# Kernel tuning notes

Hardware: AMD Instinct MI355X
Metric: run time of the kernel (lower is better)

Reference implementation:

```python
import jax, jax.numpy as jnp
import numpy as np

NUM_HEADS = 16
NEG_INF = -1e30


def setup_inputs() -> dict:
    key = jax.random.key(0)
    k1, k2, k3 = jax.random.split(key, 3)
    B, S, D = 2, 2048, 1024
    x = jax.random.normal(k1, (B, S, D), dtype=jnp.float32)
    # torch Linear(D, 3D, bias=False) stored here already transposed: y = x @ w_qkv
    w_qkv = jax.random.normal(k2, (D, 3 * D), dtype=jnp.float32) * 0.02
    w_out = jax.random.normal(k3, (D, D), dtype=jnp.float32) * 0.02
    return {"x": x, "w_qkv": w_qkv, "w_out": w_out}


def reference(x, w_qkv, w_out):
    B, S, D = x.shape
    H = NUM_HEADS
    dh = D // H
    qkv = x @ w_qkv                      # [B, S, 3D]
    q, k, v = jnp.split(qkv, 3, axis=-1)

    def to_heads(t):
        return t.reshape(B, S, H, dh).transpose(0, 2, 1, 3)  # [B, H, S, dh]

    q, k, v = to_heads(q), to_heads(k), to_heads(v)
    scale = jnp.asarray(dh, x.dtype) ** -0.5
    scores = jnp.einsum('bhqd,bhkd->bhqk', q, k) * scale     # [B, H, S, S]
    causal = jnp.tril(jnp.ones((S, S), dtype=bool))
    scores = jnp.where(causal, scores, NEG_INF)
    attn = jax.nn.softmax(scores, axis=-1)
    out = jnp.einsum('bhqk,bhkd->bhqd', attn, v)             # [B, H, S, dh]
    out = out.transpose(0, 2, 1, 3).reshape(B, S, D)
    return out @ w_out
```

## Files before the change

### kernel.cpp

```cpp
#include <hip/hip_runtime.h>

typedef unsigned short u16;
typedef unsigned int u32;

typedef __bf16 bf16x8 __attribute__((ext_vector_type(8)));
typedef _Float16 f16x8 __attribute__((ext_vector_type(8)));
typedef float f32x4 __attribute__((ext_vector_type(4)));

typedef __attribute__((address_space(1))) u32 as1_u32;
typedef __attribute__((address_space(3))) u32 as3_u32;

#define EKF 0.18033688011112042f

__device__ __forceinline__ u16 f2bf(float x) {
  u32 u = __float_as_uint(x);
  u = u + 0x7fffu + ((u >> 16) & 1u);
  return (u16)(u >> 16);
}
__device__ __forceinline__ u32 pack2(float a, float b) {
  return (u32)f2bf(a) | ((u32)f2bf(b) << 16);
}
__device__ __forceinline__ u32 pkf16(float a, float b) {
  return __builtin_bit_cast(u32, __builtin_amdgcn_cvt_pkrtz(a, b));
}
__device__ __forceinline__ u16 f2h(float a) {
  return (u16)(pkf16(a, a) & 0xffffu);
}
__device__ __forceinline__ void gld_lds16(const u16* g, const u16* l) {
  __builtin_amdgcn_global_load_lds((const as1_u32*)g, (as3_u32*)l, 16, 0, 0);
}

__global__ __launch_bounds__(256) void prepass_kernel(const float* __restrict__ x,
                                                      const float* __restrict__ w_qkv,
                                                      const float* __restrict__ w_out,
                                                      u16* __restrict__ xb,
                                                      u16* __restrict__ wqkvT,
                                                      u16* __restrict__ woutT) {
  __shared__ float tile[64][65];
  int bid = blockIdx.x;
  int t = threadIdx.x;
  if (bid < 4096) {
    int i = bid * 256 + t;
    float4 v = ((const float4*)x)[i];
    uint2 r;
    r.x = pack2(v.x, v.y);
    r.y = pack2(v.z, v.w);
    ((uint2*)xb)[i] = r;
    return;
  }
  const float* W;
  u16* WT;
  int K, N, bx, by;
  if (bid < 4096 + 768) {
    int b2 = bid - 4096;
    W = w_qkv; WT = wqkvT; K = 1024; N = 3072; bx = b2 & 15; by = b2 >> 4;
  } else {
    int b2 = bid - 4864;
    W = w_out; WT = woutT; K = 1024; N = 1024; bx = b2 & 15; by = b2 >> 4;
  }
  int k0 = bx * 64, n0 = by * 64;
  int r = t >> 4, c4 = (t & 15) * 4;
#pragma unroll
  for (int i = 0; i < 4; ++i) {
    int row = r + i * 16;
    float4 v = *(const float4*)&W[(size_t)(k0 + row) * N + n0 + c4];
    tile[row][c4 + 0] = v.x; tile[row][c4 + 1] = v.y;
    tile[row][c4 + 2] = v.z; tile[row][c4 + 3] = v.w;
  }
  __syncthreads();
#pragma unroll
  for (int i = 0; i < 4; ++i) {
    int n = r + i * 16;
    uint2 o;
    o.x = pack2(tile[c4 + 0][n], tile[c4 + 1][n]);
    o.y = pack2(tile[c4 + 2][n], tile[c4 + 3][n]);
    *(uint2*)&WT[(size_t)(n0 + n) * K + k0 + c4] = o;
  }
}

__global__ __launch_bounds__(512, 2) void gemm_qkv256_kernel(const u16* __restrict__ A,
                                                             const u16* __restrict__ BT,
                                                             u16* __restrict__ QK,
                                                             u16* __restrict__ VT) {
  __shared__ __attribute__((aligned(16))) u16 smem[65536];
  const int tid = threadIdx.x;
  const int wave = tid >> 6;
  const int lane = tid & 63;
  const int lr = lane & 15;
  const int kg = lane >> 4;
  const int l7 = lr & 7;
  const int wr = wave >> 2;
  const int wc = wave & 3;

  int b = blockIdx.x;
  int sw = (b & 7) * 24 + (b >> 3);
  const int bn = (sw % 12) * 256;
  const int bm = (sw / 12) * 256;

  const int srow = tid >> 3;
  const int scg = ((tid & 7) ^ (srow & 7)) * 8;
  const u16* pa = A + (size_t)(bm + srow) * 1024 + scg;
  const u16* pb = BT + (size_t)(bn + srow) * 1024 + scg;
  const u32 lw = (u32)wave * 512;

  f32x4 acc[8][4];
#pragma unroll
  for (int i = 0; i < 8; ++i)
#pragma unroll
    for (int j = 0; j < 4; ++j) {
      f32x4 z = {0.f, 0.f, 0.f, 0.f};
      acc[i][j] = z;
    }

  {
    u16* dA = (u16*)smem;
    u16* dB = (u16*)smem + 16384;
#pragma unroll
    for (int i = 0; i < 4; ++i) gld_lds16(pa + (size_t)(i * 64) * 1024, dA + lw + i * 4096);
#pragma unroll
    for (int i = 0; i < 4; ++i) gld_lds16(pb + (size_t)(i * 64) * 1024, dB + lw + i * 4096);
  }

  for (int t = 0; t < 16; ++t) {
    __syncthreads();
    const u16* bA = smem + (t & 1) * 32768;
    const u16* bB = bA + 16384;
    if (t + 1 < 16) {
      u16* dA = (u16*)smem + ((t + 1) & 1) * 32768;
      u16* dB = dA + 16384;
      const int k1 = (t + 1) * 64;
#pragma unroll
      for (int i = 0; i < 4; ++i) gld_lds16(pa + (size_t)(i * 64) * 1024 + k1, dA + lw + i * 4096);
#pragma unroll
      for (int i = 0; i < 4; ++i) gld_lds16(pb + (size_t)(i * 64) * 1024 + k1, dB + lw + i * 4096);
    }
    bf16x8 bfr[2][4];
#pragma unroll
    for (int kh = 0; kh < 2; ++kh)
#pragma unroll
      for (int ni = 0; ni < 4; ++ni)
        bfr[kh][ni] = *(const bf16x8*)(bB + (wc * 64 + ni * 16 + lr) * 64 +
                                       (((kh * 4 + kg) ^ l7) * 8));
#pragma unroll
    for (int ph = 0; ph < 4; ++ph) {
      const int mh = ph >> 1, kh = ph & 1;
      bf16x8 af[4];
#pragma unroll
      for (int mi = 0; mi < 4; ++mi)
        af[mi] = *(const bf16x8*)(bA + (wr * 128 + mh * 64 + mi * 16 + lr) * 64 +
                                  (((kh * 4 + kg) ^ l7) * 8));
      __builtin_amdgcn_s_barrier();
      __builtin_amdgcn_s_setprio(1);
#pragma unroll
      for (int mi = 0; mi < 4; ++mi)
#pragma unroll
        for (int ni = 0; ni < 4; ++ni)
          acc[mh * 4 + mi][ni] = __builtin_amdgcn_mfma_f32_16x16x32_bf16(
              bfr[kh][ni], af[mi], acc[mh * 4 + mi][ni], 0, 0, 0);
      __builtin_amdgcn_s_setprio(0);
      __builtin_amdgcn_s_barrier();
    }
  }

  __syncthreads();
  if (bn >= 2048) {
#pragma unroll
    for (int mi = 0; mi < 8; ++mi)
#pragma unroll
      for (int ni = 0; ni < 4; ++ni) {
        int r = bm + wr * 128 + mi * 16 + lr;
        int c = bn + wc * 64 + ni * 16 + kg * 4 - 2048;
        int bh2 = (r >> 11) * 16 + (c >> 6);
        int j = r & 2047;
        u16* vrow = VT + ((size_t)bh2 * 64 + (c & 63)) * 2048 + j;
        f32x4 a = acc[mi][ni];
#pragma unroll
        for (int rr = 0; rr < 4; ++rr) vrow[(size_t)rr * 2048] = f2h(a[rr]);
      }
  } else {
    float scale = (bn < 1024) ? EKF : 1.0f;
#pragma unroll
    for (int mi = 0; mi < 8; ++mi)
#pragma unroll
      for (int ni = 0; ni < 4; ++ni) {
        int row = wr * 128 + mi * 16 + lr;
        u32 off = (u32)row * 256 + wc * 64 + (((ni * 4 + kg) ^ (lr & 6)) * 4);
        f32x4 a = acc[mi][ni];
        *(uint2*)((u16*)smem + off) =
            make_uint2(pack2(a[0] * scale, a[1] * scale), pack2(a[2] * scale, a[3] * scale));
      }
    __syncthreads();
#pragma unroll
    for (int i = 0; i < 16; ++i) {
      int row = i * 16 + (tid >> 5);
      int lc = tid & 31;
      int blk = lc >> 3, cc = lc & 7;
      uint4 v = *(const uint4*)((const u16*)smem + (u32)row * 256 + blk * 64 +
                                (((2 * cc) ^ (row & 6)) * 4));
      *(uint4*)(QK + (size_t)(bm + row) * 2048 + bn + blk * 64 + cc * 8) = v;
    }
  }
}

__global__ __launch_bounds__(256, 2) void gemm_out_kernel(const u16* __restrict__ A,
                                                          const u16* __restrict__ BT,
                                                          float* __restrict__ C) {
  __shared__ __attribute__((aligned(16))) u16 smem[2][12288];
  const int tid = threadIdx.x;
  const int wave = tid >> 6;
  const int lane = tid & 63;
  const int lr = lane & 15;
  const int kg = lane >> 4;
  const int lr7 = lr & 7;
  const int wm = (wave >> 1) * 32;
  const int wn = (wave & 1) * 64;

  const int b = blockIdx.x;
  const int xcd = b & 7, loc = b >> 3;
  const int bm = (xcd * 8 + (loc >> 3)) * 64;
  const int bn = (loc & 7) * 128;

  const int sr = tid >> 3;
  const int scg = ((tid & 7) ^ (sr & 7)) * 8;
  const u16* pa = A + (size_t)(bm + sr) * 1024 + scg;
  const u16* pb = BT + (size_t)(bn + sr) * 1024 + scg;
  const u32 lw = (u32)wave * 512;

  f32x4 acc[2][4];
#pragma unroll
  for (int i = 0; i < 2; ++i)
#pragma unroll
    for (int j = 0; j < 4; ++j) {
      f32x4 z = {0.f, 0.f, 0.f, 0.f};
      acc[i][j] = z;
    }

  {
    u16* dA = smem[0];
    u16* dB = smem[0] + 4096;
#pragma unroll
    for (int i = 0; i < 2; ++i) gld_lds16(pa + (size_t)(i * 32) * 1024, dA + lw + i * 2048);
#pragma unroll
    for (int i = 0; i < 4; ++i) gld_lds16(pb + (size_t)(i * 32) * 1024, dB + lw + i * 2048);
  }

  for (int t = 0; t < 16; ++t) {
    __syncthreads();
    const u16* bA = smem[t & 1];
    const u16* bB = bA + 4096;
    if (t + 1 < 16) {
      u16* dA = smem[(t + 1) & 1];
      u16* dB = dA + 4096;
      const int k1 = (t + 1) * 64;
#pragma unroll
      for (int i = 0; i < 2; ++i) gld_lds16(pa + (size_t)(i * 32) * 1024 + k1, dA + lw + i * 2048);
#pragma unroll
      for (int i = 0; i < 4; ++i) gld_lds16(pb + (size_t)(i * 32) * 1024 + k1, dB + lw + i * 2048);
    }
#pragma unroll
    for (int kk = 0; kk < 2; ++kk) {
      const int ch = ((kk * 4 + kg) ^ lr7) * 8;
      bf16x8 af[2], bfr[4];
#pragma unroll
      for (int mi = 0; mi < 2; ++mi)
        af[mi] = *(const bf16x8*)(bA + (wm + mi * 16 + lr) * 64 + ch);
#pragma unroll
      for (int ni = 0; ni < 4; ++ni)
        bfr[ni] = *(const bf16x8*)(bB + (wn + ni * 16 + lr) * 64 + ch);
      __builtin_amdgcn_s_setprio(1);
#pragma unroll
      for (int mi = 0; mi < 2; ++mi)
#pragma unroll
        for (int ni = 0; ni < 4; ++ni)
          acc[mi][ni] = __builtin_amdgcn_mfma_f32_16x16x32_bf16(bfr[ni], af[mi], acc[mi][ni], 0, 0, 0);
      __builtin_amdgcn_s_setprio(0);
    }
  }

  float* buf = (float*)smem;
#pragma unroll
  for (int hc = 0; hc < 2; ++hc) {
    __syncthreads();
    if ((wave & 1) == hc) {
#pragma unroll
      for (int mi = 0; mi < 2; ++mi)
#pragma unroll
        for (int ni = 0; ni < 4; ++ni) {
          int row = wm + mi * 16 + lr;
          int cp = ((ni * 4 + kg) ^ lr) * 4;
          *(f32x4*)(buf + row * 64 + cp) = acc[mi][ni];
        }
    }
    __syncthreads();
#pragma unroll
    for (int i = 0; i < 4; ++i) {
      int row = i * 16 + (tid >> 4);
      int lc = tid & 15;
      float4 v = *(const float4*)(buf + row * 64 + ((lc ^ (row & 15)) * 4));
      *(float4*)(C + (size_t)(bm + row) * 1024 + bn + hc * 64 + lc * 4) = v;
    }
  }
}

__global__ __launch_bounds__(256, 4) void attn_mfma_kernel(const u16* __restrict__ qk,
                                                           const u16* __restrict__ vt,
                                                           u16* __restrict__ out) {
  __shared__ __attribute__((aligned(16))) u16 sK[2][64 * 64];
  __shared__ __attribute__((aligned(16))) u16 sV[2][64 * 64];
  __shared__ __attribute__((aligned(16))) u16 sP[4][16 * 64];

  const int tid = threadIdx.x;
  const int wave = tid >> 6;
  const int lane = tid & 63;
  const int lr = lane & 15;
  const int kg = lane >> 4;
  const int l7 = lr & 7;

  int idx = blockIdx.x;
  int qi = 31 - (idx >> 5);
  int bh = idx & 31;
  int b = bh >> 4, h = bh & 15;
  int q0 = qi * 64;

  const u16* qbase = qk + (size_t)b * 2048 * 2048 + h * 64;
  const u16* kbase = qbase + 1024;
  const u16* vbase = vt + (size_t)bh * 64 * 2048;
  u16* obase = out + (size_t)b * 2048 * 1024 + h * 64;

  const int sra = wave * 16 + (lane >> 3);
  const int srb = sra + 8;
  const int sc = lane & 7;
  const u32 koffA = (u32)sra * 2048 + (u32)((sc ^ (sra & 7)) * 8);
  const u32 koffB = (u32)srb * 2048 + (u32)((sc ^ (srb & 7)) * 8);
  const u32 ldsA = (wave * 2 + 0) * 512;
  const u32 ldsB = (wave * 2 + 1) * 512;

  const int qcol = q0 + wave * 16 + lr;
  bf16x8 qf0, qf1;
  {
    const u16* qrow = qbase + (size_t)qcol * 2048;
    qf0 = *(const bf16x8*)(qrow + kg * 8);
    qf1 = *(const bf16x8*)(qrow + 32 + kg * 8);
  }

  const u32 ka0 = (u32)(lr * 64 + ((kg ^ l7) * 8));
  const u32 ka1 = (u32)(lr * 64 + (((4 + kg) ^ l7) * 8));
  u16* const sPw = sP[wave];
  const u32 pr0 = (u32)(lr * 64 + (((kg * 2) ^ (l7 << 1)) * 4));
  const u32 pr1 = (u32)(lr * 64 + (((8 + kg * 2) ^ (l7 << 1)) * 4));

  f32x4 oacc[4];
#pragma unroll
  for (int i = 0; i < 4; ++i) {
    f32x4 z = {0.f, 0.f, 0.f, 0.f};
    oacc[i] = z;
  }
  float lsum = 0.f;

  const int nrounds = qi + 1;
  gld_lds16(kbase + koffA, sK[0] + ldsA);
  gld_lds16(kbase + koffB, sK[0] + ldsB);
  gld_lds16(vbase + koffA, sV[0] + ldsA);
  gld_lds16(vbase + koffB, sV[0] + ldsB);
  __syncthreads();

  for (int t = 0; t < nrounds; ++t) {
    if (t + 1 < nrounds) {
      int j1 = (t + 1) * 64;
      u16* dK = sK[(t + 1) & 1];
      u16* dV = sV[(t + 1) & 1];
      gld_lds16(kbase + (size_t)j1 * 2048 + koffA, dK + ldsA);
      gld_lds16(kbase + (size_t)j1 * 2048 + koffB, dK + ldsB);
      gld_lds16(vbase + j1 + koffA, dV + ldsA);
      gld_lds16(vbase + j1 + koffB, dV + ldsB);
    }
    const u16* sKb = sK[t & 1];
    const u16* sVb = sV[t & 1];
    const bool diag = (t == qi);

#pragma unroll
    for (int jt = 0; jt < 4; ++jt) {
      u16* pw = sPw + lr * 64 + (((jt * 4 + kg) ^ (l7 << 1)) * 4);
      if (!diag || jt <= wave) {
        bf16x8 kf0 = *(const bf16x8*)(sKb + jt * 1024 + ka0);
        bf16x8 kf1 = *(const bf16x8*)(sKb + jt * 1024 + ka1);
        f32x4 c = {0.f, 0.f, 0.f, 0.f};
        c = __builtin_amdgcn_mfma_f32_16x16x32_bf16(kf0, qf0, c, 0, 0, 0);
        c = __builtin_amdgcn_mfma_f32_16x16x32_bf16(kf1, qf1, c, 0, 0, 0);
        float p0 = exp2f(c[0]);
        float p1 = exp2f(c[1]);
        float p2 = exp2f(c[2]);
        float p3 = exp2f(c[3]);
        if (diag && jt == wave) {
          int jr = kg * 4;
          p0 = (jr + 0 <= lr) ? p0 : 0.f;
          p1 = (jr + 1 <= lr) ? p1 : 0.f;
          p2 = (jr + 2 <= lr) ? p2 : 0.f;
          p3 = (jr + 3 <= lr) ? p3 : 0.f;
        }
        lsum += (p0 + p1) + (p2 + p3);
        *(uint2*)pw = make_uint2(pkf16(p0, p1), pkf16(p2, p3));
      } else {
        *(uint2*)pw = make_uint2(0u, 0u);
      }
    }

    asm volatile("" ::: "memory");

    f16x8 pf0 = *(const f16x8*)(sPw + pr0);
    f16x8 pf1 = *(const f16x8*)(sPw + pr1);
    __builtin_amdgcn_s_setprio(1);
#pragma unroll
    for (int dt = 0; dt < 4; ++dt) {
      f16x8 vf0 = *(const f16x8*)(sVb + dt * 1024 + ka0);
      f16x8 vf1 = *(const f16x8*)(sVb + dt * 1024 + ka1);
      oacc[dt] = __builtin_amdgcn_mfma_f32_16x16x32_f16(vf0, pf0, oacc[dt], 0, 0, 0);
      oacc[dt] = __builtin_amdgcn_mfma_f32_16x16x32_f16(vf1, pf1, oacc[dt], 0, 0, 0);
    }
    __builtin_amdgcn_s_setprio(0);
    __syncthreads();
  }

  lsum += __shfl_xor(lsum, 16);
  lsum += __shfl_xor(lsum, 32);
  float inv = 1.0f / lsum;

  u16* orow = obase + (size_t)qcol * 1024;
#pragma unroll
  for (int dt = 0; dt < 4; ++dt) {
    uint2 o2 = make_uint2(pack2(oacc[dt][0] * inv, oacc[dt][1] * inv),
                          pack2(oacc[dt][2] * inv, oacc[dt][3] * inv));
    *(uint2*)(orow + dt * 16 + kg * 4) = o2;
  }
}

extern "C" void kernel_launch(void* const* d_in, const int* in_sizes, int n_in,
                              void* d_out, int out_size, void* d_ws, size_t ws_size,
                              hipStream_t stream) {
  const float* x = (const float*)d_in[0];
  const float* w_qkv = (const float*)d_in[1];
  const float* w_out = (const float*)d_in[2];
  float* out = (float*)d_out;

  char* ws = (char*)d_ws;
  u16* xb    = (u16*)(ws);
  u16* wqkvT = (u16*)(ws + (8u << 20));
  u16* woutT = (u16*)(ws + (14u << 20));
  u16* qkb   = (u16*)(ws + (16u << 20));
  u16* vtb   = (u16*)(ws + (32u << 20));
  u16* attn  = (u16*)(ws + (40u << 20));

  prepass_kernel<<<5120, 256, 0, stream>>>(x, w_qkv, w_out, xb, wqkvT, woutT);

  gemm_qkv256_kernel<<<192, 512, 0, stream>>>(xb, wqkvT, qkb, vtb);

  attn_mfma_kernel<<<1024, 256, 0, stream>>>(qkb, vtb, attn);

  gemm_out_kernel<<<512, 256, 0, stream>>>(attn, woutT, out);
}
```

Measured before the change: 163.7 us.

## Transpose P fragments in registers with permlane swaps and interleave causal tile order

```diff
diff --git a/kernel.cpp b/kernel.cpp
--- a/kernel.cpp
+++ b/kernel.cpp
@@ -6,6 +6,7 @@
 typedef __bf16 bf16x8 __attribute__((ext_vector_type(8)));
 typedef _Float16 f16x8 __attribute__((ext_vector_type(8)));
 typedef float f32x4 __attribute__((ext_vector_type(4)));
+typedef u32 u32x4 __attribute__((ext_vector_type(4)));
 
 typedef __attribute__((address_space(1))) u32 as1_u32;
 typedef __attribute__((address_space(3))) u32 as3_u32;
@@ -307,7 +308,6 @@
                                                            u16* __restrict__ out) {
   __shared__ __attribute__((aligned(16))) u16 sK[2][64 * 64];
   __shared__ __attribute__((aligned(16))) u16 sV[2][64 * 64];
-  __shared__ __attribute__((aligned(16))) u16 sP[4][16 * 64];
 
   const int tid = threadIdx.x;
   const int wave = tid >> 6;
@@ -317,7 +317,8 @@
   const int l7 = lr & 7;
 
   int idx = blockIdx.x;
-  int qi = 31 - (idx >> 5);
+  int g = idx >> 5;
+  int qi = (g & 1) ? (g >> 1) : (31 - (g >> 1));
   int bh = idx & 31;
   int b = bh >> 4, h = bh & 15;
   int q0 = qi * 64;
@@ -345,9 +346,6 @@
 
   const u32 ka0 = (u32)(lr * 64 + ((kg ^ l7) * 8));
   const u32 ka1 = (u32)(lr * 64 + (((4 + kg) ^ l7) * 8));
-  u16* const sPw = sP[wave];
-  const u32 pr0 = (u32)(lr * 64 + (((kg * 2) ^ (l7 << 1)) * 4));
-  const u32 pr1 = (u32)(lr * 64 + (((8 + kg * 2) ^ (l7 << 1)) * 4));
 
   f32x4 oacc[4];
 #pragma unroll
@@ -378,9 +376,9 @@
     const u16* sVb = sV[t & 1];
     const bool diag = (t == qi);
 
+    u32 wA0[4], wA1[4];
 #pragma unroll
     for (int jt = 0; jt < 4; ++jt) {
-      u16* pw = sPw + lr * 64 + (((jt * 4 + kg) ^ (l7 << 1)) * 4);
       if (!diag || jt <= wave) {
         bf16x8 kf0 = *(const bf16x8*)(sKb + jt * 1024 + ka0);
         bf16x8 kf1 = *(const bf16x8*)(sKb + jt * 1024 + ka1);
@@ -399,16 +397,31 @@
           p3 = (jr + 3 <= lr) ? p3 : 0.f;
         }
         lsum += (p0 + p1) + (p2 + p3);
-        *(uint2*)pw = make_uint2(pkf16(p0, p1), pkf16(p2, p3));
+        wA0[jt] = pkf16(p0, p1);
+        wA1[jt] = pkf16(p2, p3);
       } else {
-        *(uint2*)pw = make_uint2(0u, 0u);
+        wA0[jt] = 0u;
+        wA1[jt] = 0u;
       }
     }
 
-    asm volatile("" ::: "memory");
-
-    f16x8 pf0 = *(const f16x8*)(sPw + pr0);
-    f16x8 pf1 = *(const f16x8*)(sPw + pr1);
+    u32 x0 = wA0[0], y0 = wA0[1];
+    asm volatile("v_permlane32_swap_b32 %0, %1" : "+v"(x0), "+v"(y0));
+    asm volatile("v_permlane16_swap_b32 %0, %1" : "+v"(x0), "+v"(y0));
+    u32 x1 = wA1[0], y1 = wA1[1];
+    asm volatile("v_permlane32_swap_b32 %0, %1" : "+v"(x1), "+v"(y1));
+    asm volatile("v_permlane16_swap_b32 %0, %1" : "+v"(x1), "+v"(y1));
+    u32 x2 = wA0[2], y2 = wA0[3];
+    asm volatile("v_permlane32_swap_b32 %0, %1" : "+v"(x2), "+v"(y2));
+    asm volatile("v_permlane16_swap_b32 %0, %1" : "+v"(x2), "+v"(y2));
+    u32 x3 = wA1[2], y3 = wA1[3];
+    asm volatile("v_permlane32_swap_b32 %0, %1" : "+v"(x3), "+v"(y3));
+    asm volatile("v_permlane16_swap_b32 %0, %1" : "+v"(x3), "+v"(y3));
+    u32x4 pw0 = {x0, x1, y0, y1};
+    u32x4 pw1 = {x2, x3, y2, y3};
+    f16x8 pf0 = __builtin_bit_cast(f16x8, pw0);
+    f16x8 pf1 = __builtin_bit_cast(f16x8, pw1);
+
     __builtin_amdgcn_s_setprio(1);
 #pragma unroll
     for (int dt = 0; dt < 4; ++dt) {
```

New measurement: 172.3 us. 1.05x slower.
